# Kernel tuning notes

Measured on AMD Instinct MI355X. Metric: run time of the kernel, lower is better.

## Reference

```python
import jax, jax.numpy as jnp
import numpy as np

CUTOFF = 6.0   # matches init cutoff
D = 32         # descriptor/MLP width
NTYPES = 3     # len(type_map)


def setup_inputs() -> dict:
    key = jax.random.key(0)
    ks = jax.random.split(key, 13)
    b, n, m, n_ghost = 2, 8192, 64, 512
    neighbor_vectors = jax.random.normal(ks[0], (b, n, m, 4), jnp.float32)
    element_map = jax.random.randint(ks[1], (b, n), 0, NTYPES, jnp.int32)
    central_atoms = jax.random.randint(ks[2], (b, n), 0, n, jnp.int32)
    neighbor_indices = jax.random.randint(ks[3], (b, n, m), 0, n + n_ghost, jnp.int32)
    neighbor_types = jax.random.randint(ks[4], (b, n, m), 0, NTYPES, jnp.int32)
    type_embed = 0.1 * jax.random.normal(ks[5], (NTYPES, D), jnp.float32)
    elem_bias = 0.1 * jax.random.normal(ks[6], (NTYPES,), jnp.float32)
    W1 = 0.5 * jax.random.normal(ks[7], (4, D), jnp.float32)
    b1 = 0.1 * jax.random.normal(ks[8], (D,), jnp.float32)
    W2 = (1.0 / np.sqrt(D)) * jax.random.normal(ks[9], (D, D), jnp.float32)
    b2 = 0.1 * jax.random.normal(ks[10], (D,), jnp.float32)
    W3 = (1.0 / np.sqrt(D)) * jax.random.normal(ks[11], (D, 1), jnp.float32)
    b3 = 0.1 * jax.random.normal(ks[12], (1,), jnp.float32)
    return dict(element_map=element_map, central_atoms=central_atoms,
                neighbor_indices=neighbor_indices, neighbor_types=neighbor_types,
                neighbor_vectors=neighbor_vectors, n_ghost=n_ghost,
                type_embed=type_embed, elem_bias=elem_bias,
                W1=W1, b1=b1, W2=W2, b2=b2, W3=W3, b3=b3)


def _field_Ei(rel, element_map, neighbor_types, type_embed, elem_bias, W1, b1, W2, b2, W3, b3):
    # rel: [b,n,m,3] relative positions; recompute distance as the torch forward does
    dist = jnp.linalg.norm(rel, axis=-1, keepdims=True)                 # [b,n,m,1]
    fc = 0.5 * (jnp.cos(jnp.pi * jnp.minimum(dist, CUTOFF) / CUTOFF) + 1.0)
    s = jnp.exp(-dist) * fc                                             # smooth radial weight
    feat = jnp.concatenate([s, s * rel], axis=-1)                       # [b,n,m,4]
    h = jnp.tanh(feat @ W1 + b1 + type_embed[neighbor_types])           # [b,n,m,D]
    g = h.mean(axis=2)                                                  # pool over neighbors -> [b,n,D]
    h2 = jnp.tanh(g @ W2 + b2)                                          # [b,n,D]
    Ei = h2 @ W3 + b3 + elem_bias[element_map][..., None]               # [b,n,1]
    return Ei


def derive_mechanics(grad_Ei, neighbor_vectors, neighbor_indices, n_ghost):
    # grad_Ei: [b,n,m,3] = d(sum Ei)/d r_ij, with r_ij = r_j - r_i
    b, n, m, _ = grad_Ei.shape
    ntot = n + n_ghost
    bidx = jnp.arange(b)[:, None, None]
    # force on central atom i: +sum_j dE/dr_ij ; reaction scattered to neighbor j: -dE/dr_ij
    force = jnp.zeros((b, ntot, 3), grad_Ei.dtype)
    force = force.at[:, :n].add(grad_Ei.sum(axis=2))
    force = force.at[bidx, neighbor_indices].add(-grad_Ei)
    rij = neighbor_vectors[..., 1:]                                     # [b,n,m,3]
    pv = (rij[..., :, None] * grad_Ei[..., None, :]).reshape(b, n, m, 9)  # pair virial r (x) dE
    virial = pv.sum(axis=(1, 2))                                        # [b,9]
    av = jnp.zeros((b, ntot, 9), grad_Ei.dtype)
    av = av.at[bidx, neighbor_indices].add(pv)
    return force[:, :n], virial, av[:, :n]


def reference(element_map, central_atoms, neighbor_indices, neighbor_types,
              neighbor_vectors, n_ghost, type_embed, elem_bias,
              W1, b1, W2, b2, W3, b3):
    rel = neighbor_vectors[..., 1:]                                     # [b,n,m,3]

    def ei_sum(r):
        Ei = _field_Ei(r, element_map, neighbor_types, type_embed, elem_bias,
                       W1, b1, W2, b2, W3, b3)
        return Ei.sum(), Ei

    grad_Ei, Ei = jax.grad(ei_sum, has_aux=True)(rel)                   # matches autograd.grad w/ ones mask
    Etot = Ei.sum(axis=1)                                               # [b,1]
    dist = jnp.linalg.norm(rel, axis=-1, keepdims=True)
    nv = jnp.concatenate([dist, rel], axis=-1)
    force, virial, atomic_virial = derive_mechanics(grad_Ei, nv, neighbor_indices, n_ghost)
    return Etot, Ei, force, virial, atomic_virial
```

## Files before the change

kernel.cpp:

```cpp
#include <hip/hip_runtime.h>

#define CUTOFF_F 6.0f
#define PI_F 3.14159265358979323846f
#define CAP 112
#define EXCAP 8192

typedef __fp16   fp16x2 __attribute__((ext_vector_type(2)));
typedef _Float16 h2f    __attribute__((ext_vector_type(2)));

union hcv { unsigned u; fp16x2 b; h2f a; };
__device__ __forceinline__ unsigned as_u(h2f x)   { hcv c; c.a = x; return c.u; }
__device__ __forceinline__ h2f      u2a(unsigned v){ hcv c; c.u = v; return c.a; }
__device__ __forceinline__ fp16x2   u2b(unsigned v){ hcv c; c.u = v; return c.b; }

__device__ __forceinline__ unsigned pk2(float a, float b) {
  hcv c; c.b = __builtin_amdgcn_cvt_pkrtz(a, b); return c.u;
}
__device__ __forceinline__ float f16bits(unsigned v) {
  union { unsigned short u; __fp16 h; } cv; cv.u = (unsigned short)v; return (float)cv.h;
}

__device__ __forceinline__ float FDOT2(unsigned a, unsigned b, float c) {
#if defined(__has_builtin) && __has_builtin(__builtin_amdgcn_fdot2)
  return __builtin_amdgcn_fdot2(u2b(a), u2b(b), c, false);
#else
  h2f x = u2a(a), y = u2a(b);
  return fmaf((float)x.x, (float)y.x, fmaf((float)x.y, (float)y.y, c));
#endif
}

template<int CTRL>
__device__ __forceinline__ float dpp_add(float x) {
  int y = __builtin_amdgcn_update_dpp(0, __float_as_int(x), CTRL, 0xf, 0xf, true);
  return x + __int_as_float(y);
}
__device__ __forceinline__ float wave_sum63(float x) {
  x = dpp_add<0x111>(x);
  x = dpp_add<0x112>(x);
  x = dpp_add<0x114>(x);
  x = dpp_add<0x118>(x);
  x = dpp_add<0x142>(x);
  x = dpp_add<0x143>(x);
  return x;
}

__device__ __forceinline__ float fast_tanh(float x) {
  float e = __expf(2.0f * x);
  return 1.0f - 2.0f * __builtin_amdgcn_rcpf(e + 1.0f);
}

__global__ __launch_bounds__(256) void field_zero(
    int* __restrict__ counts, int* __restrict__ ecount, int bn) {
  const int i = blockIdx.x * 256 + threadIdx.x;
  if (i < bn) counts[i] = 0;
  if (i == 0) ecount[0] = 0;
}

__global__ __launch_bounds__(256) void field_main(
    const int* __restrict__ element_map,
    const int* __restrict__ neighbor_indices,
    const int* __restrict__ neighbor_types,
    const float4* __restrict__ neighbor_vectors,
    const float* __restrict__ type_embed,
    const float* __restrict__ elem_bias,
    const float* __restrict__ W1,
    const float* __restrict__ b1,
    const float* __restrict__ W2,
    const float* __restrict__ b2,
    const float* __restrict__ W3,
    const float* __restrict__ b3,
    float* __restrict__ outEi,
    int* __restrict__ counts,
    int* __restrict__ ecount,
    float4* __restrict__ extras,
    float4* __restrict__ bucket,
    float* __restrict__ partials,
    int n)
{
  __shared__ uint4  sW1f[16];
  __shared__ uint4  sW1b[16];
  __shared__ unsigned sW2h[16*33];
  __shared__ unsigned sW2d[32*17];
  __shared__ float2 sbte2[3][16];
  __shared__ float  sW3[32];
  __shared__ float  sb2[32];
  __shared__ float  sElemBias[3];
  __shared__ float  sb3;
  __shared__ float  blkEi[4];
  __shared__ float  blkVir[4][9];
  __shared__ unsigned hb[4][64][5];
  __shared__ unsigned sgp[4][16];
  __shared__ unsigned stl[4][16];
  __shared__ unsigned sdg[4][16];

  const int tid = threadIdx.x;

  if (tid < 32) { sW3[tid] = W3[tid]; sb2[tid] = b2[tid]; }
  if (tid < 16) {
    const int k0 = 2*tid, k1 = 2*tid + 1;
    sW1f[tid] = make_uint4(pk2(W1[k0],    W1[32+k0]),
                           pk2(W1[64+k0], W1[96+k0]),
                           pk2(W1[k1],    W1[32+k1]),
                           pk2(W1[64+k1], W1[96+k1]));
  } else if (tid < 32) {
    const int p = tid - 16, k0 = 2*p, k1 = 2*p + 1;
    sW1b[p] = make_uint4(pk2(W1[k0],    W1[k1]),
                         pk2(W1[32+k0], W1[32+k1]),
                         pk2(W1[64+k0], W1[64+k1]),
                         pk2(W1[96+k0], W1[96+k1]));
  } else if (tid < 80) {
    const int i = tid - 32, t = i >> 4, pp = i & 15;
    sbte2[t][pp] = make_float2(b1[2*pp]   + type_embed[t*32 + 2*pp],
                               b1[2*pp+1] + type_embed[t*32 + 2*pp+1]);
  } else if (tid == 80) {
    sb3 = b3[0];
  } else if (tid < 84) {
    sElemBias[tid - 81] = elem_bias[tid - 81];
  }
  for (int i = tid; i < 512; i += 256) {
    const int p = i >> 5, kd = i & 31;
    sW2h[p*33 + kd] = pk2(W2[(2*p)*32 + kd], W2[(2*p+1)*32 + kd]);
    const int l = i >> 4, pp = i & 15;
    sW2d[l*17 + pp] = pk2(W2[l*32 + 2*pp], W2[l*32 + 2*pp + 1]);
  }
  __syncthreads();

  const int wave = tid >> 6;
  const int lane = tid & 63;
  const int atom = blockIdx.x * 4 + wave;
  const int bb = atom / n;

  const int base = atom * 64 + lane;
  const int idx = neighbor_indices[base];
  const int dest = bb * n + idx;
  const int em = element_map[atom];

  int pos = 0;
  const bool real = (idx < n);
  if (real) pos = atomicAdd(&counts[dest], 1);

  const float4 nv = neighbor_vectors[base];
  const float rx = nv.y, ry = nv.z, rz = nv.w;
  const int typ = neighbor_types[base];

  const float d2 = rx * rx + ry * ry + rz * rz;
  const float d = sqrtf(d2);
  const float invd = (d > 0.0f) ? __builtin_amdgcn_rcpf(d) : 0.0f;
  float s, sp;
  if (d < CUTOFF_F) {
    const float arg = d * (PI_F / CUTOFF_F);
    const float cs = __cosf(arg);
    const float sn = __sinf(arg);
    const float e = __expf(-d);
    const float fc = 0.5f * (cs + 1.0f);
    const float fcp = -(0.5f * PI_F / CUTOFF_F) * sn;
    s = e * fc;
    sp = e * (fcp - fc);
  } else {
    s = 0.0f;
    sp = 0.0f;
  }
  const float f1 = s * rx, f2 = s * ry, f3 = s * rz;
  const unsigned sf01 = pk2(s, f1);
  const unsigned f23  = pk2(f2, f3);

  unsigned hpz[16];
  const int pair2 = lane & 3;
  const int grp   = lane >> 2;

#pragma unroll
  for (int P = 0; P < 4; ++P) {
#pragma unroll
    for (int e = 0; e < 4; ++e) {
      const int p = 4*P + e;
      const uint4 wq = sW1f[p];
      const float2 bt = sbte2[typ][p];
      float pre0 = FDOT2(sf01, wq.x, bt.x);
      pre0 = FDOT2(f23, wq.y, pre0);
      float pre1 = FDOT2(sf01, wq.z, bt.y);
      pre1 = FDOT2(f23, wq.w, pre1);
      const unsigned hp = pk2(fast_tanh(pre0), fast_tanh(pre1));
      hpz[p] = hp;
      hb[wave][lane][e] = hp;
    }
    h2f acc = u2a(hb[wave][grp*4 + 0][pair2]);
    acc = acc + u2a(hb[wave][grp*4 + 1][pair2]);
    acc = acc + u2a(hb[wave][grp*4 + 2][pair2]);
    acc = acc + u2a(hb[wave][grp*4 + 3][pair2]);
    acc = acc + u2a((unsigned)__shfl_xor((int)as_u(acc), 4));
    acc = acc + u2a((unsigned)__shfl_xor((int)as_u(acc), 8));
    acc = acc + u2a((unsigned)__shfl_xor((int)as_u(acc), 16));
    acc = acc + u2a((unsigned)__shfl_xor((int)as_u(acc), 32));
    if (lane < 4) {
      const h2f g2 = acc * (_Float16)(1.0f / 64.0f);
      sgp[wave][4*P + lane] = as_u(g2);
    }
  }

  const int kd = lane & 31;
  const int hh = lane >> 5;
  float acc0 = 0.0f, acc1 = 0.0f;
#pragma unroll
  for (int j = 0; j < 8; j += 2) {
    const int p = hh*8 + j;
    acc0 = FDOT2(sgp[wave][p],     sW2h[p*33 + kd],       acc0);
    acc1 = FDOT2(sgp[wave][p + 1], sW2h[(p + 1)*33 + kd], acc1);
  }
  float accs = acc0 + acc1;
  accs += __shfl_xor(accs, 32);
  accs += sb2[kd];
  const float h2v = fast_tanh(accs);
  const float tl = (1.0f - h2v * h2v) * sW3[kd];
  const float tlo = __shfl_xor(tl, 1);
  if (lane < 32 && !(kd & 1)) stl[wave][kd >> 1] = pk2(tl, tlo);

  float d0 = 0.0f, d1 = 0.0f;
#pragma unroll
  for (int j = 0; j < 8; j += 2) {
    const int p = hh*8 + j;
    d0 = FDOT2(stl[wave][p],     sW2d[kd*17 + p],     d0);
    d1 = FDOT2(stl[wave][p + 1], sW2d[kd*17 + p + 1], d1);
  }
  float dgs = (d0 + d1);
  dgs += __shfl_xor(dgs, 32);
  dgs *= (1.0f / 64.0f);
  const float dgo = __shfl_xor(dgs, 1);
  if (lane < 32 && !(kd & 1)) sdg[wave][kd >> 1] = pk2(dgs, dgo);

  const float pEi = h2v * sW3[kd];

  const h2f one16 = {(_Float16)1.0f, (_Float16)1.0f};
  float q0 = 0.0f, q1 = 0.0f, q2 = 0.0f, q3 = 0.0f;
#pragma unroll
  for (int p = 0; p < 16; ++p) {
    const h2f hp = u2a(hpz[p]);
    const h2f omh = one16 - hp * hp;
    const h2f dpre = u2a(sdg[wave][p]) * omh;
    const uint4 wq = sW1b[p];
    const unsigned du = as_u(dpre);
    q0 = FDOT2(du, wq.x, q0);
    q1 = FDOT2(du, wq.y, q1);
    q2 = FDOT2(du, wq.z, q2);
    q3 = FDOT2(du, wq.w, q3);
  }

  const float common = sp * invd * (q0 + q1 * rx + q2 * ry + q3 * rz);
  const float gx = fmaf(common, rx, s * q1);
  const float gy = fmaf(common, ry, s * q2);
  const float gz = fmaf(common, rz, s * q3);

  if (real) {
    float4 pay;
    pay.x = __uint_as_float(pk2(gx, gy));
    pay.y = __uint_as_float(pk2(gz, rx));
    pay.z = __uint_as_float(pk2(ry, rz));
    if (pos < CAP) {
      pay.w = 0.0f;
      bucket[(size_t)dest * CAP + pos] = pay;
    } else {
      const int ep = atomicAdd(ecount, 1);
      if (ep < EXCAP) { pay.w = __int_as_float(dest); extras[ep] = pay; }
    }
  }

  float sfx = wave_sum63(gx);
  float sfy = wave_sum63(gy);
  float sfz = wave_sum63(gz);
  float vr0 = wave_sum63(rx * gx), vr1 = wave_sum63(rx * gy), vr2 = wave_sum63(rx * gz);
  float vr3 = wave_sum63(ry * gx), vr4 = wave_sum63(ry * gy), vr5 = wave_sum63(ry * gz);
  float vr6 = wave_sum63(rz * gx), vr7 = wave_sum63(rz * gy), vr8 = wave_sum63(rz * gz);
  float psum = wave_sum63(pEi) * 0.5f;

  if (lane == 63) {
    const float Ei_val = psum + sb3 + sElemBias[em];
    outEi[atom] = Ei_val;
    blkEi[wave] = Ei_val;
    blkVir[wave][0] = vr0; blkVir[wave][1] = vr1; blkVir[wave][2] = vr2;
    blkVir[wave][3] = vr3; blkVir[wave][4] = vr4; blkVir[wave][5] = vr5;
    blkVir[wave][6] = vr6; blkVir[wave][7] = vr7; blkVir[wave][8] = vr8;
    float4 pay;
    pay.x = __uint_as_float(pk2(-sfx, -sfy));
    pay.y = __uint_as_float(pk2(-sfz, 0.0f));
    pay.z = 0.0f;
    const int spos = atomicAdd(&counts[atom], 1);
    if (spos < CAP) {
      pay.w = 0.0f;
      bucket[(size_t)atom * CAP + spos] = pay;
    } else {
      const int ep = atomicAdd(ecount, 1);
      if (ep < EXCAP) { pay.w = __int_as_float(atom); extras[ep] = pay; }
    }
  }

  __syncthreads();
  if (tid < 9) {
    partials[blockIdx.x * 10 + tid] =
        blkVir[0][tid] + blkVir[1][tid] + blkVir[2][tid] + blkVir[3][tid];
  } else if (tid == 9) {
    partials[blockIdx.x * 10 + 9] = blkEi[0] + blkEi[1] + blkEi[2] + blkEi[3];
  }
}

__global__ __launch_bounds__(256) void field_gather(
    const int* __restrict__ counts,
    const int* __restrict__ ecount,
    const float4* __restrict__ extras,
    const float4* __restrict__ bucket,
    const float* __restrict__ partials,
    float* __restrict__ outForce,
    float* __restrict__ outAV,
    float* __restrict__ outEtot,
    float* __restrict__ outVirial,
    int half)
{
  __shared__ float sf[4][12];
  __shared__ float sacc[4][10];
  const int tid = threadIdx.x;
  const int wave = tid >> 6;
  const int lane = tid & 63;
  const int dest = blockIdx.x * 4 + wave;

  const int rawcnt = counts[dest];
  const int cnt = (rawcnt > CAP) ? CAP : rawcnt;
  const int ec0 = *ecount;

  float fx = 0.0f, fy = 0.0f, fz = 0.0f;
  float a0 = 0, a1 = 0, a2 = 0, a3 = 0, a4 = 0, a5 = 0, a6 = 0, a7 = 0, a8 = 0;

#pragma unroll 2
  for (int l = lane; l < cnt; l += 64) {
    const float4 pay = bucket[(size_t)dest * CAP + l];
    const unsigned w0 = __float_as_uint(pay.x);
    const unsigned w1 = __float_as_uint(pay.y);
    const unsigned w2 = __float_as_uint(pay.z);
    const float gx = f16bits(w0), gy = f16bits(w0 >> 16);
    const float gz = f16bits(w1), rx = f16bits(w1 >> 16);
    const float ry = f16bits(w2), rz = f16bits(w2 >> 16);
    fx -= gx; fy -= gy; fz -= gz;
    a0 = fmaf(rx, gx, a0); a1 = fmaf(rx, gy, a1); a2 = fmaf(rx, gz, a2);
    a3 = fmaf(ry, gx, a3); a4 = fmaf(ry, gy, a4); a5 = fmaf(ry, gz, a5);
    a6 = fmaf(rz, gx, a6); a7 = fmaf(rz, gy, a7); a8 = fmaf(rz, gz, a8);
  }

  if (ec0 > 0) {
    const int ec = (ec0 < EXCAP) ? ec0 : EXCAP;
    for (int t = lane; t < ec; t += 64) {
      const float4 ex = extras[t];
      if (__float_as_int(ex.w) == dest) {
        const unsigned w0 = __float_as_uint(ex.x);
        const unsigned w1 = __float_as_uint(ex.y);
        const unsigned w2 = __float_as_uint(ex.z);
        const float gx = f16bits(w0), gy = f16bits(w0 >> 16);
        const float gz = f16bits(w1), rx = f16bits(w1 >> 16);
        const float ry = f16bits(w2), rz = f16bits(w2 >> 16);
        fx -= gx; fy -= gy; fz -= gz;
        a0 = fmaf(rx, gx, a0); a1 = fmaf(rx, gy, a1); a2 = fmaf(rx, gz, a2);
        a3 = fmaf(ry, gx, a3); a4 = fmaf(ry, gy, a4); a5 = fmaf(ry, gz, a5);
        a6 = fmaf(rz, gx, a6); a7 = fmaf(rz, gy, a7); a8 = fmaf(rz, gz, a8);
      }
    }
  }

  fx = wave_sum63(fx); fy = wave_sum63(fy); fz = wave_sum63(fz);
  a0 = wave_sum63(a0); a1 = wave_sum63(a1); a2 = wave_sum63(a2);
  a3 = wave_sum63(a3); a4 = wave_sum63(a4); a5 = wave_sum63(a5);
  a6 = wave_sum63(a6); a7 = wave_sum63(a7); a8 = wave_sum63(a8);

  if (lane == 63) {
    sf[wave][0] = fx; sf[wave][1] = fy; sf[wave][2] = fz;
    sf[wave][3] = a0; sf[wave][4] = a1; sf[wave][5] = a2;
    sf[wave][6] = a3; sf[wave][7] = a4; sf[wave][8] = a5;
    sf[wave][9] = a6; sf[wave][10] = a7; sf[wave][11] = a8;
  }
  __syncthreads();

  const int d0 = blockIdx.x * 4;
  if (tid < 12) {
    outForce[(size_t)d0 * 3 + tid] = sf[tid / 3][tid % 3];
  } else if (tid >= 64 && tid < 100) {
    const int t = tid - 64;
    outAV[(size_t)d0 * 9 + t] = sf[t / 9][3 + t % 9];
  }

  if (blockIdx.x < 2) {
    const int b = blockIdx.x;
    float acc[10] = {0, 0, 0, 0, 0, 0, 0, 0, 0, 0};
    for (int r = b * half + tid; r < (b + 1) * half; r += 256) {
#pragma unroll
      for (int t = 0; t < 10; ++t) acc[t] += partials[r * 10 + t];
    }
#pragma unroll
    for (int t = 0; t < 10; ++t) acc[t] = wave_sum63(acc[t]);
    if (lane == 63) {
#pragma unroll
      for (int t = 0; t < 10; ++t) sacc[wave][t] = acc[t];
    }
    __syncthreads();
    if (tid < 9) {
      outVirial[b * 9 + tid] = sacc[0][tid] + sacc[1][tid] + sacc[2][tid] + sacc[3][tid];
    } else if (tid == 9) {
      outEtot[b] = sacc[0][9] + sacc[1][9] + sacc[2][9] + sacc[3][9];
    }
  }
}

extern "C" void kernel_launch(void* const* d_in, const int* in_sizes, int n_in,
                              void* d_out, int out_size, void* d_ws, size_t ws_size,
                              hipStream_t stream) {
  const int* element_map        = (const int*)d_in[0];
  const int* neighbor_indices   = (const int*)d_in[2];
  const int* neighbor_types     = (const int*)d_in[3];
  const float4* neighbor_vectors = (const float4*)d_in[4];
  const float* type_embed = (const float*)d_in[6];
  const float* elem_bias  = (const float*)d_in[7];
  const float* W1 = (const float*)d_in[8];
  const float* b1 = (const float*)d_in[9];
  const float* W2 = (const float*)d_in[10];
  const float* b2 = (const float*)d_in[11];
  const float* W3 = (const float*)d_in[12];
  const float* b3 = (const float*)d_in[13];

  const int B = 2;
  const int bn = in_sizes[0];
  const int n = bn / B;
  const int nblk = bn / 4;

  float* out = (float*)d_out;
  float* outEtot   = out;
  float* outEi     = outEtot + B;
  float* outForce  = outEi + bn;
  float* outVirial = outForce + (size_t)bn * 3;
  float* outAV     = outVirial + (size_t)B * 9;

  char* ws = (char*)d_ws;
  int* counts = (int*)ws;
  size_t countBytes = (size_t)bn * sizeof(int);
  int* ecount = (int*)(ws + countBytes);
  size_t ecountBytes = 16;
  float4* extras = (float4*)(ws + countBytes + ecountBytes);
  size_t extrasBytes = (size_t)EXCAP * sizeof(float4);
  float* partials = (float*)(ws + countBytes + ecountBytes + extrasBytes);
  size_t partialBytes = (size_t)nblk * 10 * sizeof(float);
  float4* bucket = (float4*)(ws + countBytes + ecountBytes + extrasBytes + partialBytes);

  dim3 block(256);
  hipLaunchKernelGGL(field_zero, dim3((bn + 255) / 256), block, 0, stream,
                     counts, ecount, bn);
  hipLaunchKernelGGL(field_main, dim3(nblk), block, 0, stream,
                     element_map, neighbor_indices, neighbor_types,
                     neighbor_vectors, type_embed, elem_bias,
                     W1, b1, W2, b2, W3, b3,
                     outEi, counts, ecount, extras, bucket, partials, n);
  hipLaunchKernelGGL(field_gather, dim3(nblk), block, 0, stream,
                     counts, ecount, extras, bucket, partials,
                     outForce, outAV, outEtot, outVirial, nblk / B);
}
```

Measured before the change: 148.9 us.

## Partition per-atom scatter buckets and counters by XCD to cut atomic contention

Splits each destination atom's counter and bucket into 8 sub-buckets indexed by blockIdx&7, which on MI355X roughly tracks the XCD a block runs on. Atomics and bucket writes from different chiplets then land on separate cache lines, which is meant to reduce cross-XCD coherence traffic on the counters. The gather kernel reads 8 counts and loops over 8 small partitions of 24 slots each. The trade-offs are a larger zeroing pass, more bucket memory, and more overflow into the slow global extras list if one partition gets more than 24 entries.

```diff
diff --git a/kernel.cpp b/kernel.cpp
--- a/kernel.cpp
+++ b/kernel.cpp
@@ -2,7 +2,8 @@
 
 #define CUTOFF_F 6.0f
 #define PI_F 3.14159265358979323846f
-#define CAP 112
+#define CAPX 24
+#define PARTS 8
 #define EXCAP 8192
 
 typedef __fp16   fp16x2 __attribute__((ext_vector_type(2)));
@@ -50,9 +51,9 @@
 }
 
 __global__ __launch_bounds__(256) void field_zero(
-    int* __restrict__ counts, int* __restrict__ ecount, int bn) {
+    int* __restrict__ counts8, int* __restrict__ ecount, int n8) {
   const int i = blockIdx.x * 256 + threadIdx.x;
-  if (i < bn) counts[i] = 0;
+  if (i < n8) counts8[i] = 0;
   if (i == 0) ecount[0] = 0;
 }
 
@@ -70,7 +71,7 @@
     const float* __restrict__ W3,
     const float* __restrict__ b3,
     float* __restrict__ outEi,
-    int* __restrict__ counts,
+    int* __restrict__ counts8,
     int* __restrict__ ecount,
     float4* __restrict__ extras,
     float4* __restrict__ bucket,
@@ -129,6 +130,7 @@
   const int lane = tid & 63;
   const int atom = blockIdx.x * 4 + wave;
   const int bb = atom / n;
+  const int xcd = blockIdx.x & 7;
 
   const int base = atom * 64 + lane;
   const int idx = neighbor_indices[base];
@@ -137,7 +139,7 @@
 
   int pos = 0;
   const bool real = (idx < n);
-  if (real) pos = atomicAdd(&counts[dest], 1);
+  if (real) pos = atomicAdd(&counts8[dest * PARTS + xcd], 1);
 
   const float4 nv = neighbor_vectors[base];
   const float rx = nv.y, ry = nv.z, rz = nv.w;
@@ -254,9 +256,9 @@
     pay.x = __uint_as_float(pk2(gx, gy));
     pay.y = __uint_as_float(pk2(gz, rx));
     pay.z = __uint_as_float(pk2(ry, rz));
-    if (pos < CAP) {
+    if (pos < CAPX) {
       pay.w = 0.0f;
-      bucket[(size_t)dest * CAP + pos] = pay;
+      bucket[((size_t)dest * PARTS + xcd) * CAPX + pos] = pay;
     } else {
       const int ep = atomicAdd(ecount, 1);
       if (ep < EXCAP) { pay.w = __int_as_float(dest); extras[ep] = pay; }
@@ -282,10 +284,10 @@
     pay.x = __uint_as_float(pk2(-sfx, -sfy));
     pay.y = __uint_as_float(pk2(-sfz, 0.0f));
     pay.z = 0.0f;
-    const int spos = atomicAdd(&counts[atom], 1);
-    if (spos < CAP) {
+    const int spos = atomicAdd(&counts8[atom * PARTS + xcd], 1);
+    if (spos < CAPX) {
       pay.w = 0.0f;
-      bucket[(size_t)atom * CAP + spos] = pay;
+      bucket[((size_t)atom * PARTS + xcd) * CAPX + spos] = pay;
     } else {
       const int ep = atomicAdd(ecount, 1);
       if (ep < EXCAP) { pay.w = __int_as_float(atom); extras[ep] = pay; }
@@ -302,7 +304,7 @@
 }
 
 __global__ __launch_bounds__(256) void field_gather(
-    const int* __restrict__ counts,
+    const int* __restrict__ counts8,
     const int* __restrict__ ecount,
     const float4* __restrict__ extras,
     const float4* __restrict__ bucket,
@@ -320,26 +322,31 @@
   const int lane = tid & 63;
   const int dest = blockIdx.x * 4 + wave;
 
-  const int rawcnt = counts[dest];
-  const int cnt = (rawcnt > CAP) ? CAP : rawcnt;
+  const int cbase = dest * PARTS;
+  const int4 ca = *(const int4*)&counts8[cbase];
+  const int4 cb = *(const int4*)&counts8[cbase + 4];
+  const int cnts[PARTS] = {ca.x, ca.y, ca.z, ca.w, cb.x, cb.y, cb.z, cb.w};
   const int ec0 = *ecount;
 
   float fx = 0.0f, fy = 0.0f, fz = 0.0f;
   float a0 = 0, a1 = 0, a2 = 0, a3 = 0, a4 = 0, a5 = 0, a6 = 0, a7 = 0, a8 = 0;
 
-#pragma unroll 2
-  for (int l = lane; l < cnt; l += 64) {
-    const float4 pay = bucket[(size_t)dest * CAP + l];
-    const unsigned w0 = __float_as_uint(pay.x);
-    const unsigned w1 = __float_as_uint(pay.y);
-    const unsigned w2 = __float_as_uint(pay.z);
-    const float gx = f16bits(w0), gy = f16bits(w0 >> 16);
-    const float gz = f16bits(w1), rx = f16bits(w1 >> 16);
-    const float ry = f16bits(w2), rz = f16bits(w2 >> 16);
-    fx -= gx; fy -= gy; fz -= gz;
-    a0 = fmaf(rx, gx, a0); a1 = fmaf(rx, gy, a1); a2 = fmaf(rx, gz, a2);
-    a3 = fmaf(ry, gx, a3); a4 = fmaf(ry, gy, a4); a5 = fmaf(ry, gz, a5);
-    a6 = fmaf(rz, gx, a6); a7 = fmaf(rz, gy, a7); a8 = fmaf(rz, gz, a8);
+#pragma unroll
+  for (int p = 0; p < PARTS; ++p) {
+    const int cp = (cnts[p] > CAPX) ? CAPX : cnts[p];
+    if (lane < cp) {
+      const float4 pay = bucket[((size_t)cbase + p) * CAPX + lane];
+      const unsigned w0 = __float_as_uint(pay.x);
+      const unsigned w1 = __float_as_uint(pay.y);
+      const unsigned w2 = __float_as_uint(pay.z);
+      const float gx = f16bits(w0), gy = f16bits(w0 >> 16);
+      const float gz = f16bits(w1), rx = f16bits(w1 >> 16);
+      const float ry = f16bits(w2), rz = f16bits(w2 >> 16);
+      fx -= gx; fy -= gy; fz -= gz;
+      a0 = fmaf(rx, gx, a0); a1 = fmaf(rx, gy, a1); a2 = fmaf(rx, gz, a2);
+      a3 = fmaf(ry, gx, a3); a4 = fmaf(ry, gy, a4); a5 = fmaf(ry, gz, a5);
+      a6 = fmaf(rz, gx, a6); a7 = fmaf(rz, gy, a7); a8 = fmaf(rz, gz, a8);
+    }
   }
 
   if (ec0 > 0) {
@@ -433,8 +440,8 @@
   float* outAV     = outVirial + (size_t)B * 9;
 
   char* ws = (char*)d_ws;
-  int* counts = (int*)ws;
-  size_t countBytes = (size_t)bn * sizeof(int);
+  int* counts8 = (int*)ws;
+  size_t countBytes = (size_t)bn * PARTS * sizeof(int);
   int* ecount = (int*)(ws + countBytes);
   size_t ecountBytes = 16;
   float4* extras = (float4*)(ws + countBytes + ecountBytes);
@@ -444,14 +451,15 @@
   float4* bucket = (float4*)(ws + countBytes + ecountBytes + extrasBytes + partialBytes);
 
   dim3 block(256);
-  hipLaunchKernelGGL(field_zero, dim3((bn + 255) / 256), block, 0, stream,
-                     counts, ecount, bn);
+  const int n8 = bn * PARTS;
+  hipLaunchKernelGGL(field_zero, dim3((n8 + 255) / 256), block, 0, stream,
+                     counts8, ecount, n8);
   hipLaunchKernelGGL(field_main, dim3(nblk), block, 0, stream,
                      element_map, neighbor_indices, neighbor_types,
                      neighbor_vectors, type_embed, elem_bias,
                      W1, b1, W2, b2, W3, b3,
-                     outEi, counts, ecount, extras, bucket, partials, n);
+                     outEi, counts8, ecount, extras, bucket, partials, n);
   hipLaunchKernelGGL(field_gather, dim3(nblk), block, 0, stream,
-                     counts, ecount, extras, bucket, partials,
+                     counts8, ecount, extras, bucket, partials,
                      outForce, outAV, outEtot, outVirial, nblk / B);
 }
```

Result: slower. 153.2 us (+2.9%).
